# Performance work log

Measured on AMD Instinct MI355X. Metric: run time of the kernel, lower is better.

The kernel has to match this reference:

```python
import jax, jax.numpy as jnp
import numpy as np

B, S, D, H = 2, 2048, 1024, 16
HD = D // H  # head_dim = 64


def setup_inputs() -> dict:
    key = jax.random.key(0)
    ks = jax.random.split(key, 10)
    scale = 0.02
    return {
        "features": jax.random.normal(ks[0], (B, S, D), dtype=jnp.float32),
        "attention_mask": jnp.zeros((B, 1, S, S), dtype=jnp.float32),
        "wq": jax.random.normal(ks[1], (D, D), dtype=jnp.float32) * scale,
        "bq": jnp.zeros((D,), dtype=jnp.float32),
        "wk": jax.random.normal(ks[2], (D, D), dtype=jnp.float32) * scale,
        "bk": jnp.zeros((D,), dtype=jnp.float32),
        "wv": jax.random.normal(ks[3], (D, D), dtype=jnp.float32) * scale,
        "bv": jnp.zeros((D,), dtype=jnp.float32),
        "wo": jax.random.normal(ks[4], (D, D), dtype=jnp.float32) * scale,
        "bo": jnp.zeros((D,), dtype=jnp.float32),
    }


def _split_heads(x):
    # [B,S,D] -> [B,H,S,HD]
    return x.reshape(B, S, H, HD).transpose(0, 2, 1, 3)


def reference(features, attention_mask, wq, bq, wk, bk, wv, bv, wo, bo):
    scaling = HD ** -0.5
    # torch Linear: y = x @ W.T + b; Bart scales q by head_dim**-0.5
    q = _split_heads((features @ wq.T + bq) * scaling)
    k = _split_heads(features @ wk.T + bk)
    v = _split_heads(features @ wv.T + bv)
    scores = jnp.einsum("bhqd,bhkd->bhqk", q, k) + attention_mask
    attn = jax.nn.softmax(scores, axis=-1)
    ctx = jnp.einsum("bhqk,bhkd->bhqd", attn, v)
    ctx = ctx.transpose(0, 2, 1, 3).reshape(B, S, D)
    gated = ctx @ wo.T + bo
    out = features * gated
    return (out, gated)
```

## Files before the change

kernel.cpp:

```cpp
#include <hip/hip_runtime.h>

#define Bc 2
#define Sc 2048
#define Dc 1024
#define Hc 16
#define HDc 64
#define NROWS 4096
#define LOG2E 1.44269504f

typedef __attribute__((ext_vector_type(8))) _Float16 f16x8;
typedef __attribute__((ext_vector_type(4))) _Float16 f16x4;
typedef __attribute__((ext_vector_type(2))) __fp16 fp16v2;
typedef __attribute__((ext_vector_type(4))) float f32x4;
typedef __attribute__((ext_vector_type(16))) float f32x16;

__device__ __forceinline__ float ex2(float x) {
  return __builtin_amdgcn_exp2f(x);
}

__global__ __launch_bounds__(256)
void prep(const float* __restrict__ f,  const float* __restrict__ wq,
          const float* __restrict__ wk, const float* __restrict__ wv,
          const float* __restrict__ wo_,
          _Float16* __restrict__ fh, _Float16* __restrict__ wh3,
          _Float16* __restrict__ woh)
{
  int blk = blockIdx.x;
  const float* src; _Float16* hi; int base;
  if (blk < 4096)      { src = f;   hi = fh;            base = blk; }
  else if (blk < 5120) { src = wq;  hi = wh3;           base = blk - 4096; }
  else if (blk < 6144) { src = wk;  hi = wh3 + 1048576; base = blk - 5120; }
  else if (blk < 7168) { src = wv;  hi = wh3 + 2097152; base = blk - 6144; }
  else                 { src = wo_; hi = woh;           base = blk - 7168; }
  int i = base * 256 + threadIdx.x;
  float4 v = reinterpret_cast<const float4*>(src)[i];
  f16x4 h;
  h[0] = (_Float16)v.x; h[1] = (_Float16)v.y;
  h[2] = (_Float16)v.z; h[3] = (_Float16)v.w;
  reinterpret_cast<f16x4*>(hi)[i] = h;
}

__global__ __launch_bounds__(256, 4)
void gemm_qkv(const _Float16* __restrict__ Ah, const _Float16* __restrict__ Wh,
              const float* __restrict__ bq, const float* __restrict__ bk,
              const float* __restrict__ bv,
              _Float16* __restrict__ qb, _Float16* __restrict__ kb,
              _Float16* __restrict__ vtb,
              const float* __restrict__ mask, unsigned int* __restrict__ flag)
{
  __shared__ _Float16 Ash[128][40];
  __shared__ _Float16 Wsh[128][40];

  const int tid  = threadIdx.x;
  const int lane = tid & 63, wid = tid >> 6;
  const int l15  = lane & 15, l4 = lane >> 4;
  const int wr   = wid >> 1, wc = wid & 1;
  const int arow0 = blockIdx.x * 128;
  const int wrow0 = blockIdx.y * 128;

  {
    const int nthr = 768 * 256;
    int gtid = (blockIdx.y * gridDim.x + blockIdx.x) * 256 + tid;
    bool nz = false;
    for (int i = gtid; i < 2097152; i += nthr) {
      float4 mv = reinterpret_cast<const float4*>(mask)[i];
      nz = nz || (mv.x != 0.f) || (mv.y != 0.f) || (mv.z != 0.f) || (mv.w != 0.f);
    }
    if (__any(nz)) {
      if (lane == 0) atomicOr(flag, 1u);
    }
  }

  f32x4 acc[4][4];
#pragma unroll
  for (int m = 0; m < 4; ++m)
#pragma unroll
    for (int n = 0; n < 4; ++n) acc[m][n] = f32x4{0.f, 0.f, 0.f, 0.f};

  for (int k0 = 0; k0 < Dc; k0 += 32) {
    __syncthreads();
#pragma unroll
    for (int p = 0; p < 2; ++p) {
      int e = tid + 256 * p;
      int r = e >> 2, c8 = (e & 3) * 8;
      *reinterpret_cast<uint4*>(&Ash[r][c8]) =
          *reinterpret_cast<const uint4*>(Ah + (size_t)(arow0 + r) * Dc + k0 + c8);
      *reinterpret_cast<uint4*>(&Wsh[r][c8]) =
          *reinterpret_cast<const uint4*>(Wh + (size_t)(wrow0 + r) * Dc + k0 + c8);
    }
    __syncthreads();

    f16x8 bh[4];
#pragma unroll
    for (int n = 0; n < 4; ++n)
      bh[n] = *reinterpret_cast<const f16x8*>(&Wsh[wc * 64 + n * 16 + l15][l4 * 8]);
#pragma unroll
    for (int m = 0; m < 4; ++m) {
      f16x8 ah = *reinterpret_cast<const f16x8*>(&Ash[wr * 64 + m * 16 + l15][l4 * 8]);
#pragma unroll
      for (int n = 0; n < 4; ++n)
        acc[m][n] = __builtin_amdgcn_mfma_f32_16x16x32_f16(ah, bh[n], acc[m][n], 0, 0, 0);
    }
  }

#pragma unroll
  for (int m = 0; m < 4; ++m) {
#pragma unroll
    for (int n = 0; n < 4; ++n) {
      int cbase = wrow0 + wc * 64 + n * 16;
      int seg = cbase >> 10;
      int o = (cbase & 1023) + l15;
      int h = o >> 6, hd = o & 63;
      const float* bias = (seg == 0) ? bq : ((seg == 1) ? bk : bv);
      float bval = bias[o];
      float alpha = (seg == 0) ? (0.125f * LOG2E) : 1.0f;
      int r0 = arow0 + wr * 64 + m * 16 + l4 * 4;
      int b = r0 >> 11, s0 = r0 & (Sc - 1);
      if (seg == 2) {
        f16x4 pk;
#pragma unroll
        for (int reg = 0; reg < 4; ++reg)
          pk[reg] = (_Float16)((acc[m][n][reg] + bval) * alpha);
        *reinterpret_cast<f16x4*>(
            &vtb[(((size_t)b * Hc + h) * HDc + hd) * Sc + s0]) = pk;
      } else {
        _Float16* dst = (seg == 0) ? qb : kb;
#pragma unroll
        for (int reg = 0; reg < 4; ++reg) {
          float val = (acc[m][n][reg] + bval) * alpha;
          dst[(((size_t)b * Hc + h) * Sc + (s0 + reg)) * HDc + hd] = (_Float16)val;
        }
      }
    }
  }
}

__global__ __launch_bounds__(256, 4)
void gemm_wo(const _Float16* __restrict__ Ah, const _Float16* __restrict__ Wh,
             const float* __restrict__ bias,
             float* __restrict__ out0, float* __restrict__ out1,
             const float* __restrict__ feats)
{
  __shared__ _Float16 Ash[64][40];
  __shared__ _Float16 Wsh[128][40];

  const int tid  = threadIdx.x;
  const int lane = tid & 63, wid = tid >> 6;
  const int l15  = lane & 15, l4 = lane >> 4;
  const int wr   = wid >> 1, wc = wid & 1;
  const int arow0 = blockIdx.x * 64;
  const int wrow0 = blockIdx.y * 128;

  f32x4 acc[2][4];
#pragma unroll
  for (int m = 0; m < 2; ++m)
#pragma unroll
    for (int n = 0; n < 4; ++n) acc[m][n] = f32x4{0.f, 0.f, 0.f, 0.f};

  for (int k0 = 0; k0 < Dc; k0 += 32) {
    __syncthreads();
    {
      int r = tid >> 2, c8 = (tid & 3) * 8;
      *reinterpret_cast<uint4*>(&Ash[r][c8]) =
          *reinterpret_cast<const uint4*>(Ah + (size_t)(arow0 + r) * Dc + k0 + c8);
    }
#pragma unroll
    for (int p = 0; p < 2; ++p) {
      int e = tid + 256 * p;
      int r = e >> 2, c8 = (e & 3) * 8;
      *reinterpret_cast<uint4*>(&Wsh[r][c8]) =
          *reinterpret_cast<const uint4*>(Wh + (size_t)(wrow0 + r) * Dc + k0 + c8);
    }
    __syncthreads();

    f16x8 bh[4];
#pragma unroll
    for (int n = 0; n < 4; ++n)
      bh[n] = *reinterpret_cast<const f16x8*>(&Wsh[wc * 64 + n * 16 + l15][l4 * 8]);
#pragma unroll
    for (int m = 0; m < 2; ++m) {
      f16x8 ah = *reinterpret_cast<const f16x8*>(&Ash[wr * 32 + m * 16 + l15][l4 * 8]);
#pragma unroll
      for (int n = 0; n < 4; ++n)
        acc[m][n] = __builtin_amdgcn_mfma_f32_16x16x32_f16(ah, bh[n], acc[m][n], 0, 0, 0);
    }
  }

#pragma unroll
  for (int m = 0; m < 2; ++m) {
#pragma unroll
    for (int n = 0; n < 4; ++n) {
      int c = wrow0 + wc * 64 + n * 16 + l15;
      float bval = bias[c];
#pragma unroll
      for (int reg = 0; reg < 4; ++reg) {
        int r = arow0 + wr * 32 + m * 16 + l4 * 4 + reg;
        float val = acc[m][n][reg] + bval;
        out1[(size_t)r * Dc + c] = val;
        out0[(size_t)r * Dc + c] = feats[(size_t)r * Dc + c] * val;
      }
    }
  }
}

#define QB 128
#define KB 64
#define NT (Sc / KB)

__global__ __launch_bounds__(256, 2)
void attn_mfma(const _Float16* __restrict__ q,
               const _Float16* __restrict__ k,
               const _Float16* __restrict__ vt,
               const float* __restrict__ mask,
               const unsigned int* __restrict__ mflag,
               _Float16* __restrict__ ctxh)
{
  __shared__ _Float16 Ks[2][KB * 64];
  __shared__ _Float16 Vs[2][HDc * 64];

  const int tid  = threadIdx.x;
  const int lane = tid & 63;
  const int wq   = tid >> 6;
  const int l31  = lane & 31;
  const int hi   = lane >> 5;

  const int nqb  = Sc / QB;
  const int bid  = blockIdx.x;
  const int swz  = (bid & 7) * 64 + (bid >> 3);
  const int head = swz / nqb;
  const int q0   = (swz % nqb) * QB;
  const int b    = head / Hc;
  const int h    = head % Hc;

  const bool use_mask = (*mflag != 0u);

  const _Float16* kbase  = k  + (size_t)head * Sc * HDc;
  const _Float16* vtbase = vt + (size_t)head * HDc * Sc;
  const _Float16* qbase  = q  + ((size_t)head * Sc + q0 + wq * 32 + l31) * HDc;
  const float*    ml     = mask + ((size_t)b * Sc + q0 + wq * 32 + l31) * Sc + 4 * hi;

  const int r0s = tid >> 3, cs = tid & 7;
  const int r1s = r0s + 32;
  const int so0 = r0s * 64 + ((cs ^ (r0s & 7)) * 8);
  const int so1 = r1s * 64 + ((cs ^ (r1s & 7)) * 8);

  f16x8 qf[4];
#pragma unroll
  for (int c = 0; c < 4; ++c)
    qf[c] = *reinterpret_cast<const f16x8*>(qbase + hi * 8 + 16 * c);

  f16x8 ones;
#pragma unroll
  for (int i = 0; i < 8; ++i) ones[i] = (_Float16)1.0f;

  f32x16 O0, O1, lacc;
#pragma unroll
  for (int i = 0; i < 16; ++i) { O0[i] = 0.f; O1[i] = 0.f; lacc[i] = 0.f; }
  float m_q = -3e38f;

  *reinterpret_cast<uint4*>(&Ks[0][so0]) =
      *reinterpret_cast<const uint4*>(kbase + (size_t)r0s * HDc + cs * 8);
  *reinterpret_cast<uint4*>(&Ks[0][so1]) =
      *reinterpret_cast<const uint4*>(kbase + (size_t)r1s * HDc + cs * 8);
  *reinterpret_cast<uint4*>(&Vs[0][so0]) =
      *reinterpret_cast<const uint4*>(vtbase + (size_t)r0s * Sc + cs * 8);
  *reinterpret_cast<uint4*>(&Vs[0][so1]) =
      *reinterpret_cast<const uint4*>(vtbase + (size_t)r1s * Sc + cs * 8);
  float4 mpf[8];
  if (use_mask) {
#pragma unroll
    for (int t2 = 0; t2 < 2; ++t2)
#pragma unroll
      for (int j = 0; j < 4; ++j)
        mpf[t2 * 4 + j] = *reinterpret_cast<const float4*>(ml + 32 * t2 + 8 * j);
  }

  for (int kt = 0; kt < NT; ++kt) {
    const int k0 = kt * KB;
    const int cur = kt & 1, nxt = cur ^ 1;
    __syncthreads();

    uint4 kr0, kr1, vr0, vr1;
    const bool pf = (kt + 1) < NT;
    if (pf) {
      const int k1 = k0 + KB;
      kr0 = *reinterpret_cast<const uint4*>(kbase + (size_t)(k1 + r0s) * HDc + cs * 8);
      kr1 = *reinterpret_cast<const uint4*>(kbase + (size_t)(k1 + r1s) * HDc + cs * 8);
      vr0 = *reinterpret_cast<const uint4*>(vtbase + (size_t)r0s * Sc + k1 + cs * 8);
      vr1 = *reinterpret_cast<const uint4*>(vtbase + (size_t)r1s * Sc + k1 + cs * 8);
    }

    f32x16 s[2];
    __builtin_amdgcn_s_setprio(1);
#pragma unroll
    for (int t2 = 0; t2 < 2; ++t2) {
      f32x16 acc;
#pragma unroll
      for (int i = 0; i < 16; ++i) acc[i] = 0.f;
      const int krow = t2 * 32 + l31;
#pragma unroll
      for (int c = 0; c < 4; ++c) {
        const int ofs = krow * 64 + (((2 * c + hi) ^ (krow & 7)) * 8);
        acc = __builtin_amdgcn_mfma_f32_32x32x16_f16(
            *reinterpret_cast<const f16x8*>(&Ks[cur][ofs]), qf[c], acc, 0, 0, 0);
      }
      s[t2] = acc;
    }
    __builtin_amdgcn_s_setprio(0);

    if (use_mask) {
#pragma unroll
      for (int t2 = 0; t2 < 2; ++t2)
#pragma unroll
        for (int j = 0; j < 4; ++j) {
          float4 mv = mpf[t2 * 4 + j];
          s[t2][4 * j + 0] += mv.x * LOG2E; s[t2][4 * j + 1] += mv.y * LOG2E;
          s[t2][4 * j + 2] += mv.z * LOG2E; s[t2][4 * j + 3] += mv.w * LOG2E;
        }
      if (pf) {
#pragma unroll
        for (int t2 = 0; t2 < 2; ++t2)
#pragma unroll
          for (int j = 0; j < 4; ++j)
            mpf[t2 * 4 + j] = *reinterpret_cast<const float4*>(
                ml + (k0 + KB) + 32 * t2 + 8 * j);
      }
    }

    float t0_[8];
#pragma unroll
    for (int i = 0; i < 8; ++i)
      t0_[i] = fmaxf(fmaxf(s[0][2 * i], s[0][2 * i + 1]),
                     fmaxf(s[1][2 * i], s[1][2 * i + 1]));
    float t1_0 = fmaxf(fmaxf(t0_[0], t0_[1]), fmaxf(t0_[2], t0_[3]));
    float t1_1 = fmaxf(fmaxf(t0_[4], t0_[5]), fmaxf(t0_[6], t0_[7]));
    float lm = fmaxf(t1_0, t1_1);

    if (!__all(lm - m_q <= 8.0f * LOG2E)) {
      float vm = fmaxf(lm, __shfl_xor(lm, 32));
      float mn = fmaxf(m_q, vm);
      float cc = ex2(m_q - mn);
      m_q = mn;
#pragma unroll
      for (int reg = 0; reg < 16; ++reg) {
        int q_r = (reg & 3) + 8 * (reg >> 2) + 4 * hi;
        float ccr = __shfl(cc, q_r);
        O0[reg] *= ccr; O1[reg] *= ccr; lacc[reg] *= ccr;
      }
    }

    __builtin_amdgcn_s_setprio(1);
#pragma unroll
    for (int c = 0; c < 4; ++c) {
      const int t2 = c >> 1, rb = (c & 1) * 8;
      float p0 = ex2(s[t2][rb + 0] - m_q);
      float p1 = ex2(s[t2][rb + 1] - m_q);
      float p2 = ex2(s[t2][rb + 2] - m_q);
      float p3 = ex2(s[t2][rb + 3] - m_q);
      float p4 = ex2(s[t2][rb + 4] - m_q);
      float p5 = ex2(s[t2][rb + 5] - m_q);
      float p6 = ex2(s[t2][rb + 6] - m_q);
      float p7 = ex2(s[t2][rb + 7] - m_q);
      union { fp16v2 h; unsigned int u; } w0, w1, w2, w3;
      w0.h = __builtin_amdgcn_cvt_pkrtz(p0, p1);
      w1.h = __builtin_amdgcn_cvt_pkrtz(p2, p3);
      w2.h = __builtin_amdgcn_cvt_pkrtz(p4, p5);
      w3.h = __builtin_amdgcn_cvt_pkrtz(p6, p7);
      unsigned int u0 = w0.u, u1 = w1.u, u2 = w2.u, u3 = w3.u;
      asm("v_permlane32_swap_b32 %0, %1" : "+v"(u0), "+v"(u2));
      asm("v_permlane32_swap_b32 %0, %1" : "+v"(u1), "+v"(u3));
      union { unsigned int u[4]; f16x8 f; } pa;
      pa.u[0] = u0; pa.u[1] = u1; pa.u[2] = u2; pa.u[3] = u3;

      lacc = __builtin_amdgcn_mfma_f32_32x32x16_f16(pa.f, ones, lacc, 0, 0, 0);
      const int vofs = l31 * 64 + (((2 * c + hi) ^ (l31 & 7)) * 8);
      O0 = __builtin_amdgcn_mfma_f32_32x32x16_f16(
          pa.f, *reinterpret_cast<const f16x8*>(&Vs[cur][vofs]), O0, 0, 0, 0);
      O1 = __builtin_amdgcn_mfma_f32_32x32x16_f16(
          pa.f, *reinterpret_cast<const f16x8*>(&Vs[cur][vofs + 32 * 64]), O1, 0, 0, 0);
    }
    __builtin_amdgcn_s_setprio(0);

    if (pf) {
      *reinterpret_cast<uint4*>(&Ks[nxt][so0]) = kr0;
      *reinterpret_cast<uint4*>(&Ks[nxt][so1]) = kr1;
      *reinterpret_cast<uint4*>(&Vs[nxt][so0]) = vr0;
      *reinterpret_cast<uint4*>(&Vs[nxt][so1]) = vr1;
    }
  }

#pragma unroll
  for (int reg = 0; reg < 16; ++reg) {
    int q_r = (reg & 3) + 8 * (reg >> 2) + 4 * hi;
    float inv = 1.0f / lacc[reg];
    size_t rowbase = ((size_t)b * Sc + (q0 + wq * 32 + q_r)) * Dc + h * HDc;
    ctxh[rowbase + l31]      = (_Float16)(O0[reg] * inv);
    ctxh[rowbase + 32 + l31] = (_Float16)(O1[reg] * inv);
  }
}

extern "C" void kernel_launch(void* const* d_in, const int* in_sizes, int n_in,
                              void* d_out, int out_size, void* d_ws, size_t ws_size,
                              hipStream_t stream) {
  const float* feats = (const float*)d_in[0];
  const float* mask  = (const float*)d_in[1];
  const float* wq    = (const float*)d_in[2];
  const float* bq    = (const float*)d_in[3];
  const float* wk    = (const float*)d_in[4];
  const float* bk    = (const float*)d_in[5];
  const float* wv    = (const float*)d_in[6];
  const float* bv    = (const float*)d_in[7];
  const float* wo    = (const float*)d_in[8];
  const float* bo    = (const float*)d_in[9];

  char* ws = (char*)d_ws;
  const size_t MB = (size_t)1 << 20;
  _Float16* fh    = (_Float16*)(ws);
  _Float16* wh3   = (_Float16*)(ws + 8  * MB);
  _Float16* woh   = (_Float16*)(ws + 14 * MB);
  _Float16* qb    = (_Float16*)(ws + 16 * MB);
  _Float16* kb    = (_Float16*)(ws + 24 * MB);
  _Float16* vtb   = (_Float16*)(ws + 32 * MB);
  _Float16* ctxh  = (_Float16*)(ws + 40 * MB);
  unsigned int* mflag = (unsigned int*)(ws + 48 * MB);

  float* out   = (float*)d_out;
  float* gated = out + 4194304;

  (void)hipMemsetAsync(mflag, 0, 4, stream);

  prep<<<8192, 256, 0, stream>>>(feats, wq, wk, wv, wo, fh, wh3, woh);

  gemm_qkv<<<dim3(NROWS / 128, 3072 / 128), 256, 0, stream>>>(
      fh, wh3, bq, bk, bv, qb, kb, vtb, mask, mflag);

  attn_mfma<<<Bc * Hc * (Sc / QB), 256, 0, stream>>>(qb, kb, vtb, mask, mflag, ctxh);

  gemm_wo<<<dim3(NROWS / 64, Dc / 128), 256, 0, stream>>>(
      ctxh, woh, bo, out, gated, feats);
}
```

Baseline: 146.6 us.

## Split attention KV range across two wave groups and merge partial softmax in LDS

The attention kernel now runs 512 threads per block. Two halves of four waves each process the same 128 query rows over separate halves of the key/value sequence, each with its own double-buffered LDS tiles. At the end, partial max, row sums and output accumulators are exchanged through LDS that is unioned with the KV buffers, and combined with flash-decoding style rescaling. This doubles waves per query block to hide latency and raise occupancy on a grid of only 512 blocks. The cost is an extra epilogue reduction, more LDS per block, and an occupancy hint of 4 blocks per CU that may constrain registers.

Result: slower. 209.4 us (+42.9%).

```diff
diff --git a/kernel.cpp b/kernel.cpp
--- a/kernel.cpp
+++ b/kernel.cpp
@@ -205,9 +205,9 @@
 
 #define QB 128
 #define KB 64
-#define NT (Sc / KB)
-
-__global__ __launch_bounds__(256, 2)
+#define NTH 16
+
+__global__ __launch_bounds__(512, 4)
 void attn_mfma(const _Float16* __restrict__ q,
                const _Float16* __restrict__ k,
                const _Float16* __restrict__ vt,
@@ -215,12 +215,17 @@
                const unsigned int* __restrict__ mflag,
                _Float16* __restrict__ ctxh)
 {
-  __shared__ _Float16 Ks[2][KB * 64];
-  __shared__ _Float16 Vs[2][HDc * 64];
+  __shared__ union {
+    struct { _Float16 K[2][2][KB * 64]; _Float16 V[2][2][HDc * 64]; } kv;
+    struct { float O[4][32][64]; float m0[4][32]; float l0_[4][32];
+             float m1[4][32]; float l1_[4][32]; } ep;
+  } sm;
 
   const int tid  = threadIdx.x;
   const int lane = tid & 63;
-  const int wq   = tid >> 6;
+  const int wq8  = tid >> 6;
+  const int g    = wq8 & 3;
+  const int half = wq8 >> 2;
   const int l31  = lane & 31;
   const int hi   = lane >> 5;
 
@@ -231,15 +236,18 @@
   const int q0   = (swz % nqb) * QB;
   const int b    = head / Hc;
   const int h    = head % Hc;
+  const int kvb  = half * (Sc / 2);
 
   const bool use_mask = (*mflag != 0u);
 
   const _Float16* kbase  = k  + (size_t)head * Sc * HDc;
   const _Float16* vtbase = vt + (size_t)head * HDc * Sc;
-  const _Float16* qbase  = q  + ((size_t)head * Sc + q0 + wq * 32 + l31) * HDc;
-  const float*    ml     = mask + ((size_t)b * Sc + q0 + wq * 32 + l31) * Sc + 4 * hi;
-
-  const int r0s = tid >> 3, cs = tid & 7;
+  const _Float16* qbase  = q  + ((size_t)head * Sc + q0 + g * 32 + l31) * HDc;
+  const float*    mlh    = mask + ((size_t)b * Sc + q0 + g * 32 + l31) * Sc
+                           + kvb + 4 * hi;
+
+  const int tidh = tid & 255;
+  const int r0s = tidh >> 3, cs = tidh & 7;
   const int r1s = r0s + 32;
   const int so0 = r0s * 64 + ((cs ^ (r0s & 7)) * 8);
   const int so1 = r1s * 64 + ((cs ^ (r1s & 7)) * 8);
@@ -258,32 +266,32 @@
   for (int i = 0; i < 16; ++i) { O0[i] = 0.f; O1[i] = 0.f; lacc[i] = 0.f; }
   float m_q = -3e38f;
 
-  *reinterpret_cast<uint4*>(&Ks[0][so0]) =
-      *reinterpret_cast<const uint4*>(kbase + (size_t)r0s * HDc + cs * 8);
-  *reinterpret_cast<uint4*>(&Ks[0][so1]) =
-      *reinterpret_cast<const uint4*>(kbase + (size_t)r1s * HDc + cs * 8);
-  *reinterpret_cast<uint4*>(&Vs[0][so0]) =
-      *reinterpret_cast<const uint4*>(vtbase + (size_t)r0s * Sc + cs * 8);
-  *reinterpret_cast<uint4*>(&Vs[0][so1]) =
-      *reinterpret_cast<const uint4*>(vtbase + (size_t)r1s * Sc + cs * 8);
+  *reinterpret_cast<uint4*>(&sm.kv.K[half][0][so0]) =
+      *reinterpret_cast<const uint4*>(kbase + (size_t)(kvb + r0s) * HDc + cs * 8);
+  *reinterpret_cast<uint4*>(&sm.kv.K[half][0][so1]) =
+      *reinterpret_cast<const uint4*>(kbase + (size_t)(kvb + r1s) * HDc + cs * 8);
+  *reinterpret_cast<uint4*>(&sm.kv.V[half][0][so0]) =
+      *reinterpret_cast<const uint4*>(vtbase + (size_t)r0s * Sc + kvb + cs * 8);
+  *reinterpret_cast<uint4*>(&sm.kv.V[half][0][so1]) =
+      *reinterpret_cast<const uint4*>(vtbase + (size_t)r1s * Sc + kvb + cs * 8);
   float4 mpf[8];
   if (use_mask) {
 #pragma unroll
     for (int t2 = 0; t2 < 2; ++t2)
 #pragma unroll
       for (int j = 0; j < 4; ++j)
-        mpf[t2 * 4 + j] = *reinterpret_cast<const float4*>(ml + 32 * t2 + 8 * j);
-  }
-
-  for (int kt = 0; kt < NT; ++kt) {
+        mpf[t2 * 4 + j] = *reinterpret_cast<const float4*>(mlh + 32 * t2 + 8 * j);
+  }
+
+  for (int kt = 0; kt < NTH; ++kt) {
     const int k0 = kt * KB;
     const int cur = kt & 1, nxt = cur ^ 1;
     __syncthreads();
 
     uint4 kr0, kr1, vr0, vr1;
-    const bool pf = (kt + 1) < NT;
+    const bool pf = (kt + 1) < NTH;
     if (pf) {
-      const int k1 = k0 + KB;
+      const int k1 = kvb + k0 + KB;
       kr0 = *reinterpret_cast<const uint4*>(kbase + (size_t)(k1 + r0s) * HDc + cs * 8);
       kr1 = *reinterpret_cast<const uint4*>(kbase + (size_t)(k1 + r1s) * HDc + cs * 8);
       vr0 = *reinterpret_cast<const uint4*>(vtbase + (size_t)r0s * Sc + k1 + cs * 8);
@@ -302,7 +310,8 @@
       for (int c = 0; c < 4; ++c) {
         const int ofs = krow * 64 + (((2 * c + hi) ^ (krow & 7)) * 8);
         acc = __builtin_amdgcn_mfma_f32_32x32x16_f16(
-            *reinterpret_cast<const f16x8*>(&Ks[cur][ofs]), qf[c], acc, 0, 0, 0);
+            *reinterpret_cast<const f16x8*>(&sm.kv.K[half][cur][ofs]), qf[c],
+            acc, 0, 0, 0);
       }
       s[t2] = acc;
     }
@@ -323,7 +332,7 @@
 #pragma unroll
           for (int j = 0; j < 4; ++j)
             mpf[t2 * 4 + j] = *reinterpret_cast<const float4*>(
-                ml + (k0 + KB) + 32 * t2 + 8 * j);
+                mlh + (k0 + KB) + 32 * t2 + 8 * j);
       }
     }
 
@@ -375,27 +384,61 @@
       lacc = __builtin_amdgcn_mfma_f32_32x32x16_f16(pa.f, ones, lacc, 0, 0, 0);
       const int vofs = l31 * 64 + (((2 * c + hi) ^ (l31 & 7)) * 8);
       O0 = __builtin_amdgcn_mfma_f32_32x32x16_f16(
-          pa.f, *reinterpret_cast<const f16x8*>(&Vs[cur][vofs]), O0, 0, 0, 0);
+          pa.f, *reinterpret_cast<const f16x8*>(&sm.kv.V[half][cur][vofs]),
+          O0, 0, 0, 0);
       O1 = __builtin_amdgcn_mfma_f32_32x32x16_f16(
-          pa.f, *reinterpret_cast<const f16x8*>(&Vs[cur][vofs + 32 * 64]), O1, 0, 0, 0);
+          pa.f, *reinterpret_cast<const f16x8*>(&sm.kv.V[half][cur][vofs + 32 * 64]),
+          O1, 0, 0, 0);
     }
     __builtin_amdgcn_s_setprio(0);
 
     if (pf) {
-      *reinterpret_cast<uint4*>(&Ks[nxt][so0]) = kr0;
-      *reinterpret_cast<uint4*>(&Ks[nxt][so1]) = kr1;
-      *reinterpret_cast<uint4*>(&Vs[nxt][so0]) = vr0;
-      *reinterpret_cast<uint4*>(&Vs[nxt][so1]) = vr1;
-    }
-  }
-
-#pragma unroll
-  for (int reg = 0; reg < 16; ++reg) {
-    int q_r = (reg & 3) + 8 * (reg >> 2) + 4 * hi;
-    float inv = 1.0f / lacc[reg];
-    size_t rowbase = ((size_t)b * Sc + (q0 + wq * 32 + q_r)) * Dc + h * HDc;
-    ctxh[rowbase + l31]      = (_Float16)(O0[reg] * inv);
-    ctxh[rowbase + 32 + l31] = (_Float16)(O1[reg] * inv);
+      *reinterpret_cast<uint4*>(&sm.kv.K[half][nxt][so0]) = kr0;
+      *reinterpret_cast<uint4*>(&sm.kv.K[half][nxt][so1]) = kr1;
+      *reinterpret_cast<uint4*>(&sm.kv.V[half][nxt][so0]) = vr0;
+      *reinterpret_cast<uint4*>(&sm.kv.V[half][nxt][so1]) = vr1;
+    }
+  }
+
+  __syncthreads();
+
+  if (hi == 0) {
+    if (half == 0) sm.ep.m0[g][l31] = m_q; else sm.ep.m1[g][l31] = m_q;
+  }
+  if (l31 == 0) {
+#pragma unroll
+    for (int reg = 0; reg < 16; ++reg) {
+      int q_r = (reg & 3) + 8 * (reg >> 2) + 4 * hi;
+      if (half == 0) sm.ep.l0_[g][q_r] = lacc[reg];
+      else           sm.ep.l1_[g][q_r] = lacc[reg];
+    }
+  }
+  if (half == 1) {
+#pragma unroll
+    for (int reg = 0; reg < 16; ++reg) {
+      int q_r = (reg & 3) + 8 * (reg >> 2) + 4 * hi;
+      sm.ep.O[g][q_r][l31]      = O0[reg];
+      sm.ep.O[g][q_r][32 + l31] = O1[reg];
+    }
+  }
+  __syncthreads();
+
+  if (half == 0) {
+#pragma unroll
+    for (int reg = 0; reg < 16; ++reg) {
+      int q_r = (reg & 3) + 8 * (reg >> 2) + 4 * hi;
+      float m0v = sm.ep.m0[g][q_r], m1v = sm.ep.m1[g][q_r];
+      float l0v = lacc[reg],        l1v = sm.ep.l1_[g][q_r];
+      float mm = fmaxf(m0v, m1v);
+      float e0 = ex2(m0v - mm), e1 = ex2(m1v - mm);
+      float inv = 1.0f / (l0v * e0 + l1v * e1);
+      int row = q0 + g * 32 + q_r;
+      size_t base = ((size_t)b * Sc + row) * Dc + h * HDc;
+      ctxh[base + l31] =
+          (_Float16)((O0[reg] * e0 + sm.ep.O[g][q_r][l31] * e1) * inv);
+      ctxh[base + 32 + l31] =
+          (_Float16)((O1[reg] * e0 + sm.ep.O[g][q_r][32 + l31] * e1) * inv);
+    }
   }
 }
 
@@ -434,7 +477,7 @@
   gemm_qkv<<<dim3(NROWS / 128, 3072 / 128), 256, 0, stream>>>(
       fh, wh3, bq, bk, bv, qb, kb, vtb, mask, mflag);
 
-  attn_mfma<<<Bc * Hc * (Sc / QB), 256, 0, stream>>>(qb, kb, vtb, mask, mflag, ctxh);
+  attn_mfma<<<Bc * Hc * (Sc / QB), 512, 0, stream>>>(qb, kb, vtb, mask, mflag, ctxh);
 
   gemm_wo<<<dim3(NROWS / 64, Dc / 128), 256, 0, stream>>>(
       ctxh, woh, bo, out, gated, feats);
```
